# Optimization experiments

Measured on AMD Instinct MI355X. Metric: run time of the kernel, lower is better.

Reference implementation:

```python
import jax, jax.numpy as jnp
import numpy as np

SIZE = 768
SMALL = SIZE // 4 + 1  # 193
N_ROWS = 16 * 512      # 8192 flattened timesteps
N_CODES = 30000
N_PAIRS = 300000


def setup_inputs() -> dict:
    key = jax.random.key(0)
    ks = jax.random.split(key, 10)
    rnn_output = jax.random.normal(ks[0], (16, 512, SIZE), dtype=jnp.float32)
    weight = jax.random.normal(ks[1], (N_CODES, SIZE + 1), dtype=jnp.float32) * 0.02
    weight1 = jax.random.normal(ks[2], (N_CODES, SMALL), dtype=jnp.float32) * 0.02
    idx0 = jnp.stack([
        jax.random.randint(ks[3], (N_PAIRS,), 0, N_ROWS),
        jax.random.randint(ks[4], (N_PAIRS,), 0, N_CODES),
    ], axis=1).astype(jnp.int64)
    y0 = (jax.random.uniform(ks[5], (N_PAIRS,)) < 0.5).astype(jnp.float32)
    idx1 = jnp.stack([
        jax.random.randint(ks[6], (N_PAIRS,), 0, N_ROWS),
        jax.random.randint(ks[7], (N_PAIRS,), 0, N_CODES),
    ], axis=1).astype(jnp.int64)
    y1 = (jax.random.uniform(ks[8], (N_PAIRS,)) < 0.5).astype(jnp.float32)
    seen0 = jnp.zeros((N_PAIRS,), dtype=jnp.float32)
    seen1 = jnp.zeros((N_PAIRS,), dtype=jnp.float32)
    return {"rnn_output": rnn_output, "weight": weight, "weight1": weight1,
            "idx0": idx0, "y0": y0, "seen0": seen0,
            "idx1": idx1, "y1": y1, "seen1": seen1}


def _embedding_dot(features, table, idx):
    # gather feature rows and code-embedding rows, then row-wise dot -> [N]
    f = features[idx[:, 0]]   # [N, D]
    w = table[idx[:, 1]]      # [N, D]
    return jnp.sum(f * w, axis=-1)


def _bce_logits_sum(logits, targets):
    # stable: log(1 + exp(x)) - x*y, summed
    return jnp.sum(jnp.logaddexp(jnp.float32(0.0), logits) - logits * targets)


def reference(rnn_output, weight, weight1, idx0, y0, seen0, idx1, y1, seen1):
    flat = rnn_output.reshape(-1, SIZE)                     # [B*T, size]
    bias = jnp.ones((flat.shape[0], 1), dtype=flat.dtype)
    rnn_with_bias = jnp.concatenate([flat, bias], axis=1)   # [B*T, size+1]

    final = _embedding_dot(rnn_with_bias, weight, idx0)     # [N]
    loss = _bce_logits_sum(final, y0)

    smaller = rnn_with_bias[:, -SMALL:]                     # [B*T, small]
    final1 = _embedding_dot(smaller, weight1, idx1)         # [N]
    loss1 = _bce_logits_sum(final1, y1)

    return final, loss + loss1
```

## Files before the change

kernel.cpp:

```cpp
#include <hip/hip_runtime.h>
#include <hip/hip_fp16.h>

#define FSIZE   768
#define TW0     769
#define TW1     193
#define COL1    576
#define NPAIRS  300000
#define NCODES  30000
#define NROWS   8192
#define NCB     32768

#define NWAVES0 (NPAIRS / 32)
#define NB0     2344
#define NB1     1176
#define NGRID   (NB0 + NB1)
#define NPART   NGRID

#define NBF     3072
#define NBW0    11250
#define NBW1    2813
#define NBH     2344
#define PRE_S1  (NBF)
#define PRE_S2  (NBF + NBW0)
#define PRE_S3  (NBF + NBW0 + NBW1)
#define NPRE    (NBF + NBW0 + NBW1 + NBH)

#define O_FEAT8  ((size_t)0)
#define O_W08    (O_FEAT8 + 1572864)
#define O_W18    (O_W08 + 5760000)
#define O_B0F    (O_W18 + 1440000)
#define O_B1F    (O_B0F + 30000)
#define O_CNT    (O_B1F + 30000)
#define O_CUR    (O_CNT + 65536)
#define O_SREC   (O_CUR + 65536)
#define O_PART   (O_SREC + 2400000)
#define WS_U32   (O_PART + NPART + 64)

#define FSCALE   16.0f
#define WSCALE   64.0f
#define DESCALE  (1.0f / 1024.0f)

typedef float f32x2_t __attribute__((ext_vector_type(2)));

__device__ __forceinline__ float loss_term(float x, float y) {
    float ax = fabsf(x);
    return fmaxf(x, 0.0f) + log1pf(__expf(-ax)) - x * y;
}

__device__ __forceinline__ float4 ld4u(const float* p) {
    float4 v; __builtin_memcpy(&v, p, 16); return v;
}

#if defined(__has_builtin)
# if __has_builtin(__builtin_amdgcn_cvt_pk_f32_fp8)
#  define HW_FP8_DEC 1
# endif
# if __has_builtin(__builtin_amdgcn_cvt_pk_fp8_f32)
#  define HW_FP8_ENC 1
# endif
#endif

__device__ __forceinline__ float sw_fp8_to_f32(unsigned b) {
    unsigned mag = b & 0x7fu;
    unsigned r = ((b & 0x80u) << 24) | ((mag << 20) + 0x3C000000u);
    float f = __uint_as_float(r);
    return mag ? f : 0.0f;
}

template <bool HI>
__device__ __forceinline__ f32x2_t fp8x2_to_f32(unsigned u) {
#ifdef HW_FP8_DEC
    return __builtin_amdgcn_cvt_pk_f32_fp8(u, HI);
#else
    f32x2_t o;
    unsigned lo8 = HI ? ((u >> 16) & 0xffu) : (u & 0xffu);
    unsigned hi8 = HI ? ((u >> 24) & 0xffu) : ((u >> 8) & 0xffu);
    o[0] = sw_fp8_to_f32(lo8);
    o[1] = sw_fp8_to_f32(hi8);
    return o;
#endif
}

__device__ __forceinline__ unsigned sw_f32_to_fp8(float x) {
    unsigned short h = __half_as_ushort(__float2half(x));
    unsigned s = ((unsigned)h >> 8) & 0x80u;
    int e = (h >> 10) & 31;
    unsigned m = h & 1023u;
    if (e >= 23) return s | 0x7eu;
    if (e < 9)  return s;
    unsigned t = ((unsigned)(e - 8) << 3) | (m >> 7);
    unsigned rnd = (m >> 6) & 1u, sticky = (m & 63u) ? 1u : 0u;
    t += (rnd & (sticky | (t & 1u)));
    if (t > 0x7eu) t = 0x7eu;
    return s | t;
}

__device__ __forceinline__ unsigned f32x4_to_fp8(float a, float b, float c, float d) {
#ifdef HW_FP8_ENC
    int u = __builtin_amdgcn_cvt_pk_fp8_f32(a, b, 0, false);
    u = __builtin_amdgcn_cvt_pk_fp8_f32(c, d, u, true);
    return (unsigned)u;
#else
    return sw_f32_to_fp8(a) | (sw_f32_to_fp8(b) << 8)
         | (sw_f32_to_fp8(c) << 16) | (sw_f32_to_fp8(d) << 24);
#endif
}

__device__ __forceinline__ float dot16(uint4 u, const float* w, float s) {
    f32x2_t p;
    p = fp8x2_to_f32<false>(u.x); s += p[0] * w[0]  + p[1] * w[1];
    p = fp8x2_to_f32<true >(u.x); s += p[0] * w[2]  + p[1] * w[3];
    p = fp8x2_to_f32<false>(u.y); s += p[0] * w[4]  + p[1] * w[5];
    p = fp8x2_to_f32<true >(u.y); s += p[0] * w[6]  + p[1] * w[7];
    p = fp8x2_to_f32<false>(u.z); s += p[0] * w[8]  + p[1] * w[9];
    p = fp8x2_to_f32<true >(u.z); s += p[0] * w[10] + p[1] * w[11];
    p = fp8x2_to_f32<false>(u.w); s += p[0] * w[12] + p[1] * w[13];
    p = fp8x2_to_f32<true >(u.w); s += p[0] * w[14] + p[1] * w[15];
    return s;
}

__device__ __forceinline__ float dot8(uint2 u, const float* w, float s) {
    f32x2_t p;
    p = fp8x2_to_f32<false>(u.x); s += p[0] * w[0] + p[1] * w[1];
    p = fp8x2_to_f32<true >(u.x); s += p[0] * w[2] + p[1] * w[3];
    p = fp8x2_to_f32<false>(u.y); s += p[0] * w[4] + p[1] * w[5];
    p = fp8x2_to_f32<true >(u.y); s += p[0] * w[6] + p[1] * w[7];
    return s;
}

__device__ __forceinline__ void unpack16(uint4 u, float* w) {
    f32x2_t p;
    p = fp8x2_to_f32<false>(u.x); w[0]  = p[0]; w[1]  = p[1];
    p = fp8x2_to_f32<true >(u.x); w[2]  = p[0]; w[3]  = p[1];
    p = fp8x2_to_f32<false>(u.y); w[4]  = p[0]; w[5]  = p[1];
    p = fp8x2_to_f32<true >(u.y); w[6]  = p[0]; w[7]  = p[1];
    p = fp8x2_to_f32<false>(u.z); w[8]  = p[0]; w[9]  = p[1];
    p = fp8x2_to_f32<true >(u.z); w[10] = p[0]; w[11] = p[1];
    p = fp8x2_to_f32<false>(u.w); w[12] = p[0]; w[13] = p[1];
    p = fp8x2_to_f32<true >(u.w); w[14] = p[0]; w[15] = p[1];
}

__device__ __forceinline__ void unpack8(uint2 u, float* w) {
    f32x2_t p;
    p = fp8x2_to_f32<false>(u.x); w[0] = p[0]; w[1] = p[1];
    p = fp8x2_to_f32<true >(u.x); w[2] = p[0]; w[3] = p[1];
    p = fp8x2_to_f32<false>(u.y); w[4] = p[0]; w[5] = p[1];
    p = fp8x2_to_f32<true >(u.y); w[6] = p[0]; w[7] = p[1];
}

__global__ __launch_bounds__(256) void zero_cnt_kernel(int* __restrict__ cnt) {
    cnt[blockIdx.x * 256 + threadIdx.x] = 0;
}

__global__ __launch_bounds__(256) void fused_pre_kernel(
    const float* __restrict__ feat, const float* __restrict__ w0,
    const float* __restrict__ w1,
    const int* __restrict__ idx0, const int* __restrict__ idx1,
    uint2* __restrict__ feat8, uint2* __restrict__ w08, uint2* __restrict__ w18,
    float* __restrict__ b0f, float* __restrict__ b1f, int* __restrict__ cnt)
{
    const int bid = blockIdx.x;
    if (bid < PRE_S1) {
        const int t = bid * 256 + threadIdx.x;
        const float* src = feat + (size_t)t * 8;
        float4 a = *(const float4*)src, b = *(const float4*)(src + 4);
        uint2 o;
        o.x = f32x4_to_fp8(a.x * FSCALE, a.y * FSCALE, a.z * FSCALE, a.w * FSCALE);
        o.y = f32x4_to_fp8(b.x * FSCALE, b.y * FSCALE, b.z * FSCALE, b.w * FSCALE);
        feat8[t] = o;
    } else if (bid < PRE_S2) {
        const int t = (bid - PRE_S1) * 256 + threadIdx.x;
        const int c = t / 96;
        const int e = (t - c * 96) * 8;
        const float* src = w0 + (size_t)c * TW0 + e;
        float4 a = ld4u(src), b = ld4u(src + 4);
        uint2 o;
        o.x = f32x4_to_fp8(a.x * WSCALE, a.y * WSCALE, a.z * WSCALE, a.w * WSCALE);
        o.y = f32x4_to_fp8(b.x * WSCALE, b.y * WSCALE, b.z * WSCALE, b.w * WSCALE);
        w08[t] = o;
        if (e == 0) b0f[c] = w0[(size_t)c * TW0 + FSIZE];
    } else if (bid < PRE_S3) {
        const int t = (bid - PRE_S2) * 256 + threadIdx.x;
        if (t < NCODES * 24) {
            const int c = t / 24;
            const int e = (t - c * 24) * 8;
            const float* src = w1 + (size_t)c * TW1 + e;
            float4 a = ld4u(src), b = ld4u(src + 4);
            uint2 o;
            o.x = f32x4_to_fp8(a.x * WSCALE, a.y * WSCALE, a.z * WSCALE, a.w * WSCALE);
            o.y = f32x4_to_fp8(b.x * WSCALE, b.y * WSCALE, b.z * WSCALE, b.w * WSCALE);
            w18[t] = o;
            if (e == 0) b1f[c] = w1[(size_t)c * TW1 + (TW1 - 1)];
        }
    } else {
        const int t = (bid - PRE_S3) * 256 + threadIdx.x;
        if (t < 2 * NPAIRS) {
            if (t < NPAIRS) atomicAdd(&cnt[idx0[2 * t + 1]], 1);
            else            atomicAdd(&cnt[NCB + idx1[2 * (t - NPAIRS) + 1]], 1);
        }
    }
}

__global__ __launch_bounds__(1024) void scan2_kernel(const int* __restrict__ cnt,
                                                     int* __restrict__ cursor) {
    __shared__ int wsum[16];
    __shared__ int wbase[16];
    const int t = threadIdx.x;
    const int lane = t & 63, wv = t >> 6;
    const int4* c4 = (const int4*)cnt + (size_t)t * 16;
    int4 v[16];
#pragma unroll
    for (int j = 0; j < 16; ++j) v[j] = c4[j];
    int s = 0;
#pragma unroll
    for (int j = 0; j < 16; ++j) {
        int a;
        a = v[j].x; v[j].x = s; s += a;
        a = v[j].y; v[j].y = s; s += a;
        a = v[j].z; v[j].z = s; s += a;
        a = v[j].w; v[j].w = s; s += a;
    }
    int incl = s;
#pragma unroll
    for (int off = 1; off < 64; off <<= 1) {
        int u = __shfl_up(incl, off, 64);
        if (lane >= off) incl += u;
    }
    if (lane == 63) wsum[wv] = incl;
    __syncthreads();
    if (wv == 0 && lane < 16) {
        int mysum = wsum[lane];
        int winc = mysum;
#pragma unroll
        for (int off = 1; off < 16; off <<= 1) {
            int u = __shfl_up(winc, off, 64);
            if (lane >= off) winc += u;
        }
        wbase[lane] = winc - mysum;
    }
    __syncthreads();
    const int base = wbase[wv] + incl - s;
    int4* cu = (int4*)cursor + (size_t)t * 16;
#pragma unroll
    for (int j = 0; j < 16; ++j)
        cu[j] = make_int4(base + v[j].x, base + v[j].y, base + v[j].z, base + v[j].w);
}

__global__ __launch_bounds__(256) void scatter2_kernel(
    const int* __restrict__ idx0, const float* __restrict__ y0,
    const int* __restrict__ idx1, const float* __restrict__ y1,
    int* __restrict__ cursor, uint4* __restrict__ srec)
{
    const int t = blockIdx.x * 256 + threadIdx.x;
    if (t < NPAIRS) {
        int r = idx0[2 * t], c = idx0[2 * t + 1];
        int pos = atomicAdd(&cursor[c], 1);
        srec[pos] = make_uint4((unsigned)r, (unsigned)c, __float_as_uint(y0[t]), (unsigned)t);
    } else if (t < 2 * NPAIRS) {
        int p = t - NPAIRS;
        int r = idx1[2 * p], c = idx1[2 * p + 1];
        int pos = atomicAdd(&cursor[NCB + c], 1);
        srec[pos] = make_uint4((unsigned)r, (unsigned)c, __float_as_uint(y1[p]), (unsigned)p);
    }
}

__global__ __launch_bounds__(256) void main3_kernel(
    const unsigned char* __restrict__ feat8, const unsigned char* __restrict__ w08,
    const unsigned char* __restrict__ w18,
    const float* __restrict__ b0f, const float* __restrict__ b1f,
    const uint4* __restrict__ srec,
    float* __restrict__ out_final, float* __restrict__ partial)
{
    __shared__ float bsum[4];
    const int lane = threadIdx.x & 63;
    const int wv   = threadIdx.x >> 6;
    float wavesum = 0.f;

    if (blockIdx.x < NB0) {
        const int work = (blockIdx.x & 7) * (NB0 / 8) + (blockIdx.x >> 3);
        const int wid = work * 4 + wv;
        if (wid < NWAVES0) {
            const int g = lane >> 4, sub = lane & 15;
            const uint4 rec = srec[(size_t)wid * 32 + 8 * g + (sub & 7)];
            int prev_c = -1;
            float wc[48];
            float wb = 0.f, lg = 0.f;
#pragma unroll
            for (int j = 0; j < 8; ++j) {
                const int src = (lane & 48) | j;
                const int r = __shfl((int)rec.x, src, 64);
                const int c = __shfl((int)rec.y, src, 64);
                if (c != prev_c) {
                    prev_c = c;
                    const unsigned char* wr = w08 + (size_t)c * FSIZE + 48 * sub;
                    uint4 wu0 = *(const uint4*)wr;
                    uint4 wu1 = *(const uint4*)(wr + 16);
                    uint4 wu2 = *(const uint4*)(wr + 32);
                    unpack16(wu0, &wc[0]);
                    unpack16(wu1, &wc[16]);
                    unpack16(wu2, &wc[32]);
                    wb = b0f[c];
                }
                const unsigned char* fr = feat8 + (size_t)r * FSIZE + 48 * sub;
                uint4 f0 = *(const uint4*)fr;
                uint4 f1 = *(const uint4*)(fr + 16);
                uint4 f2 = *(const uint4*)(fr + 32);
                float s = dot16(f0, &wc[0], 0.f);
                s = dot16(f1, &wc[16], s);
                s = dot16(f2, &wc[32], s);
                s += __shfl_xor(s, 8, 64);
                s += __shfl_xor(s, 4, 64);
                s += __shfl_xor(s, 2, 64);
                s += __shfl_xor(s, 1, 64);
                lg = (sub == j) ? s * DESCALE + wb : lg;
            }
            float ll = 0.f;
            if (sub < 8) {
                out_final[rec.w] = lg;
                ll = loss_term(lg, __uint_as_float(rec.z));
            }
#pragma unroll
            for (int m = 32; m; m >>= 1) ll += __shfl_xor(ll, m, 64);
            wavesum = ll;
        }
    } else {
        const int tb = blockIdx.x - NB0;
        const int work1 = (tb & 7) * (NB1 / 8) + (tb >> 3);
        const long base = (long)(work1 * 4 + wv) * 64;
        if (base < NPAIRS) {
            const int g = lane >> 3, sub = lane & 7;
            long lpos = base + 8 * g + sub;
            if (lpos > NPAIRS - 1) lpos = NPAIRS - 1;
            const uint4 rec = srec[(size_t)NPAIRS + lpos];
            int prev_c = -1;
            float wc[24];
            float wb = 0.f, lg = 0.f;
#pragma unroll
            for (int j = 0; j < 8; ++j) {
                const bool valid = (base + 8 * g + j) < NPAIRS;
                const int src = (lane & 56) | j;
                const int r = __shfl((int)rec.x, src, 64);
                const int c = __shfl((int)rec.y, src, 64);
                if (valid) {
                    if (c != prev_c) {
                        prev_c = c;
                        const unsigned char* wr = w18 + (size_t)c * 192 + 24 * sub;
                        uint2 wu0 = *(const uint2*)wr;
                        uint2 wu1 = *(const uint2*)(wr + 8);
                        uint2 wu2 = *(const uint2*)(wr + 16);
                        unpack8(wu0, &wc[0]);
                        unpack8(wu1, &wc[8]);
                        unpack8(wu2, &wc[16]);
                        wb = b1f[c];
                    }
                    const unsigned char* fr = feat8 + (size_t)r * FSIZE + COL1 + 24 * sub;
                    uint2 f0 = *(const uint2*)fr;
                    uint2 f1 = *(const uint2*)(fr + 8);
                    uint2 f2 = *(const uint2*)(fr + 16);
                    float s = dot8(f0, &wc[0], 0.f);
                    s = dot8(f1, &wc[8], s);
                    s = dot8(f2, &wc[16], s);
                    s += __shfl_xor(s, 4, 64);
                    s += __shfl_xor(s, 2, 64);
                    s += __shfl_xor(s, 1, 64);
                    lg = (sub == j) ? s * DESCALE + wb : lg;
                }
            }
            float ll = 0.f;
            if ((base + 8 * g + sub) < NPAIRS)
                ll = loss_term(lg, __uint_as_float(rec.z));
#pragma unroll
            for (int m = 32; m; m >>= 1) ll += __shfl_xor(ll, m, 64);
            wavesum = ll;
        }
    }

    if (lane == 0) bsum[wv] = wavesum;
    __syncthreads();
    if (threadIdx.x == 0)
        partial[blockIdx.x] = bsum[0] + bsum[1] + bsum[2] + bsum[3];
}

__global__ __launch_bounds__(1024) void reduce_kernel(
    const float* __restrict__ partial, int n, float* __restrict__ out)
{
    __shared__ float sh[1024];
    float s = 0.0f;
    for (int i = threadIdx.x; i < n; i += 1024) s += partial[i];
    sh[threadIdx.x] = s;
    __syncthreads();
    for (int off = 512; off; off >>= 1) {
        if ((int)threadIdx.x < off) sh[threadIdx.x] += sh[threadIdx.x + off];
        __syncthreads();
    }
    if (threadIdx.x == 0) out[0] = sh[0];
}

__global__ __launch_bounds__(256) void task0_kernel(
    const float* __restrict__ feat, const float* __restrict__ wt,
    const int* __restrict__ idx, const float* __restrict__ y,
    float* __restrict__ out_final, float* __restrict__ partial)
{
    __shared__ float lsum[4];
    const int lane = threadIdx.x & 63;
    const int wv = threadIdx.x >> 6;
    const int pair = blockIdx.x * 4 + wv;
    const int r = idx[2 * pair];
    const int c = idx[2 * pair + 1];
    const float4* f4 = (const float4*)(feat + (size_t)r * FSIZE);
    const float* wrow = wt + (size_t)c * TW0;
    float s = 0.0f;
#pragma unroll
    for (int k = 0; k < 3; ++k) {
        const int j = lane + (k << 6);
        float4 f = f4[j];
        float4 w = ld4u(wrow + 4 * j);
        s += f.x * w.x + f.y * w.y + f.z * w.z + f.w * w.w;
    }
#pragma unroll
    for (int m = 32; m; m >>= 1) s += __shfl_xor(s, m, 64);
    if (lane == 0) {
        const float logit = s + wrow[FSIZE];
        out_final[pair] = logit;
        lsum[wv] = loss_term(logit, y[pair]);
    }
    __syncthreads();
    if (threadIdx.x == 0)
        partial[blockIdx.x] = lsum[0] + lsum[1] + lsum[2] + lsum[3];
}

__global__ __launch_bounds__(256) void task1_kernel(
    const float* __restrict__ feat, const float* __restrict__ wt,
    const int* __restrict__ idx, const float* __restrict__ y,
    float* __restrict__ partial)
{
    __shared__ float lsum[16];
    const int lane = threadIdx.x & 63;
    const int wv = threadIdx.x >> 6;
    const int sub = lane & 15;
    const int pg = lane >> 4;
    const int pair = (blockIdx.x * 4 + wv) * 4 + pg;
    const int r = idx[2 * pair];
    const int c = idx[2 * pair + 1];
    const float4* f4 = (const float4*)(feat + (size_t)r * FSIZE + COL1);
    const float* wrow = wt + (size_t)c * TW1;
    float s = 0.0f;
#pragma unroll
    for (int k = 0; k < 3; ++k) {
        const int j = sub + (k << 4);
        float4 f = f4[j];
        float4 w = ld4u(wrow + 4 * j);
        s += f.x * w.x + f.y * w.y + f.z * w.z + f.w * w.w;
    }
#pragma unroll
    for (int m = 8; m; m >>= 1) s += __shfl_xor(s, m, 64);
    if (sub == 0) {
        const float logit = s + wrow[TW1 - 1];
        lsum[wv * 4 + pg] = loss_term(logit, y[pair]);
    }
    __syncthreads();
    if (threadIdx.x == 0) {
        float t = 0.0f;
#pragma unroll
        for (int i = 0; i < 16; ++i) t += lsum[i];
        partial[blockIdx.x] = t;
    }
}

extern "C" void kernel_launch(void* const* d_in, const int* in_sizes, int n_in,
                              void* d_out, int out_size, void* d_ws, size_t ws_size,
                              hipStream_t stream) {
    const float* feat = (const float*)d_in[0];
    const float* w0   = (const float*)d_in[1];
    const float* w1   = (const float*)d_in[2];
    const int*   idx0 = (const int*)d_in[3];
    const float* y0   = (const float*)d_in[4];
    const int*   idx1 = (const int*)d_in[6];
    const float* y1   = (const float*)d_in[7];

    float* out = (float*)d_out;
    unsigned* ws = (unsigned*)d_ws;

    if (ws_size >= WS_U32 * 4) {
        unsigned char* feat8 = (unsigned char*)(ws + O_FEAT8);
        unsigned char* w08   = (unsigned char*)(ws + O_W08);
        unsigned char* w18   = (unsigned char*)(ws + O_W18);
        float* b0f   = (float*)(ws + O_B0F);
        float* b1f   = (float*)(ws + O_B1F);
        int*   cnt   = (int*)(ws + O_CNT);
        int*   cursor= (int*)(ws + O_CUR);
        uint4* srec  = (uint4*)(ws + O_SREC);
        float* part  = (float*)(ws + O_PART);

        zero_cnt_kernel<<<256, 256, 0, stream>>>(cnt);
        fused_pre_kernel<<<NPRE, 256, 0, stream>>>(
            feat, w0, w1, idx0, idx1,
            (uint2*)feat8, (uint2*)w08, (uint2*)w18, b0f, b1f, cnt);
        scan2_kernel<<<1, 1024, 0, stream>>>(cnt, cursor);
        scatter2_kernel<<<(2 * NPAIRS + 255) / 256, 256, 0, stream>>>(
            idx0, y0, idx1, y1, cursor, srec);
        main3_kernel<<<NGRID, 256, 0, stream>>>(
            feat8, w08, w18, b0f, b1f, srec, out, part);
        reduce_kernel<<<1, 1024, 0, stream>>>(part, NPART, out + NPAIRS);
    } else {
        float* part = (float*)ws;
        const int nb0 = NPAIRS / 4;
        const int nb1 = NPAIRS / 16;
        task0_kernel<<<nb0, 256, 0, stream>>>(feat, w0, idx0, y0, out, part);
        task1_kernel<<<nb1, 256, 0, stream>>>(feat, w1, idx1, y1, part + nb0);
        reduce_kernel<<<1, 1024, 0, stream>>>(part, nb0 + nb1, out + NPAIRS);
    }
}
```

Measured before the change: 161.3 us.

## Widen fp8 packing, grid-stride prep kernels, enlarge task0 waves, fold loss reduce into atomics

The prep kernel now encodes 16 values per thread into uint4 and uses a fixed, smaller grid with per-thread loops, and the histogram section is moved first. The scatter kernel also uses grid-stride loops and zeroes the loss output. The task0 path in main3 now has each wave handle 64 pairs with all 16 lanes per group active, which halves its block count. The final reduce kernel is removed and replaced by per-block atomicAdd into the loss. Together these cut launch count and block scheduling overhead, at the cost of higher register pressure and a nondeterministic float summation order.

```diff
diff --git a/kernel.cpp b/kernel.cpp
--- a/kernel.cpp
+++ b/kernel.cpp
@@ -10,20 +10,22 @@
 #define NROWS   8192
 #define NCB     32768
 
-#define NWAVES0 (NPAIRS / 32)
-#define NB0     2344
+#define NB0     1176
 #define NB1     1176
 #define NGRID   (NB0 + NB1)
 #define NPART   NGRID
 
-#define NBF     3072
-#define NBW0    11250
-#define NBW1    2813
-#define NBH     2344
-#define PRE_S1  (NBF)
-#define PRE_S2  (NBF + NBW0)
-#define PRE_S3  (NBF + NBW0 + NBW1)
-#define NPRE    (NBF + NBW0 + NBW1 + NBH)
+#define PB_H    512
+#define PB_F    512
+#define PB_W0   1024
+#define PB_W1   256
+#define NPRE    (PB_H + PB_F + PB_W0 + PB_W1)
+#define S_H     (PB_H)
+#define S_F     (PB_H + PB_F)
+#define S_W0    (PB_H + PB_F + PB_W0)
+#define FEAT_U4 393216
+#define W0_U4   1440000
+#define W1_U4   360000
 
 #define O_FEAT8  ((size_t)0)
 #define O_W08    (O_FEAT8 + 1572864)
@@ -106,6 +108,16 @@
 #endif
 }
 
+__device__ __forceinline__ uint4 enc16(const float* s, float sc) {
+    float4 a = ld4u(s), b = ld4u(s + 4), c = ld4u(s + 8), d = ld4u(s + 12);
+    uint4 o;
+    o.x = f32x4_to_fp8(a.x * sc, a.y * sc, a.z * sc, a.w * sc);
+    o.y = f32x4_to_fp8(b.x * sc, b.y * sc, b.z * sc, b.w * sc);
+    o.z = f32x4_to_fp8(c.x * sc, c.y * sc, c.z * sc, c.w * sc);
+    o.w = f32x4_to_fp8(d.x * sc, d.y * sc, d.z * sc, d.w * sc);
+    return o;
+}
+
 __device__ __forceinline__ float dot16(uint4 u, const float* w, float s) {
     f32x2_t p;
     p = fp8x2_to_f32<false>(u.x); s += p[0] * w[0]  + p[1] * w[1];
@@ -156,47 +168,52 @@
     const float* __restrict__ feat, const float* __restrict__ w0,
     const float* __restrict__ w1,
     const int* __restrict__ idx0, const int* __restrict__ idx1,
-    uint2* __restrict__ feat8, uint2* __restrict__ w08, uint2* __restrict__ w18,
+    uint4* __restrict__ feat8, uint4* __restrict__ w08, uint4* __restrict__ w18,
     float* __restrict__ b0f, float* __restrict__ b1f, int* __restrict__ cnt)
 {
     const int bid = blockIdx.x;
-    if (bid < PRE_S1) {
-        const int t = bid * 256 + threadIdx.x;
-        const float* src = feat + (size_t)t * 8;
-        float4 a = *(const float4*)src, b = *(const float4*)(src + 4);
-        uint2 o;
-        o.x = f32x4_to_fp8(a.x * FSCALE, a.y * FSCALE, a.z * FSCALE, a.w * FSCALE);
-        o.y = f32x4_to_fp8(b.x * FSCALE, b.y * FSCALE, b.z * FSCALE, b.w * FSCALE);
-        feat8[t] = o;
-    } else if (bid < PRE_S2) {
-        const int t = (bid - PRE_S1) * 256 + threadIdx.x;
-        const int c = t / 96;
-        const int e = (t - c * 96) * 8;
-        const float* src = w0 + (size_t)c * TW0 + e;
-        float4 a = ld4u(src), b = ld4u(src + 4);
-        uint2 o;
-        o.x = f32x4_to_fp8(a.x * WSCALE, a.y * WSCALE, a.z * WSCALE, a.w * WSCALE);
-        o.y = f32x4_to_fp8(b.x * WSCALE, b.y * WSCALE, b.z * WSCALE, b.w * WSCALE);
-        w08[t] = o;
-        if (e == 0) b0f[c] = w0[(size_t)c * TW0 + FSIZE];
-    } else if (bid < PRE_S3) {
-        const int t = (bid - PRE_S2) * 256 + threadIdx.x;
-        if (t < NCODES * 24) {
-            const int c = t / 24;
-            const int e = (t - c * 24) * 8;
-            const float* src = w1 + (size_t)c * TW1 + e;
-            float4 a = ld4u(src), b = ld4u(src + 4);
-            uint2 o;
-            o.x = f32x4_to_fp8(a.x * WSCALE, a.y * WSCALE, a.z * WSCALE, a.w * WSCALE);
-            o.y = f32x4_to_fp8(b.x * WSCALE, b.y * WSCALE, b.z * WSCALE, b.w * WSCALE);
-            w18[t] = o;
-            if (e == 0) b1f[c] = w1[(size_t)c * TW1 + (TW1 - 1)];
+    if (bid < S_H) {
+        const int tid = bid * 256 + threadIdx.x;
+#pragma unroll
+        for (int k = 0; k < 5; ++k) {
+            const int i = tid + k * (PB_H * 256);
+            if (i < 2 * NPAIRS) {
+                if (i < NPAIRS) atomicAdd(&cnt[idx0[2 * i + 1]], 1);
+                else            atomicAdd(&cnt[NCB + idx1[2 * (i - NPAIRS) + 1]], 1);
+            }
+        }
+    } else if (bid < S_F) {
+        const int tid = (bid - S_H) * 256 + threadIdx.x;
+#pragma unroll
+        for (int k = 0; k < 3; ++k) {
+            const int i = tid + k * (PB_F * 256);
+            feat8[i] = enc16(feat + (size_t)i * 16, FSCALE);
+        }
+    } else if (bid < S_W0) {
+        const int tid = (bid - S_F) * 256 + threadIdx.x;
+#pragma unroll
+        for (int k = 0; k < 6; ++k) {
+            const int i = tid + k * (PB_W0 * 256);
+            if (i < W0_U4) {
+                const int c = i / 48;
+                const int e = (i - c * 48) * 16;
+                const float* src = w0 + (size_t)c * TW0 + e;
+                w08[i] = enc16(src, WSCALE);
+                if (e == 0) b0f[c] = src[FSIZE];
+            }
         }
     } else {
-        const int t = (bid - PRE_S3) * 256 + threadIdx.x;
-        if (t < 2 * NPAIRS) {
-            if (t < NPAIRS) atomicAdd(&cnt[idx0[2 * t + 1]], 1);
-            else            atomicAdd(&cnt[NCB + idx1[2 * (t - NPAIRS) + 1]], 1);
+        const int tid = (bid - S_W0) * 256 + threadIdx.x;
+#pragma unroll
+        for (int k = 0; k < 6; ++k) {
+            const int i = tid + k * (PB_W1 * 256);
+            if (i < W1_U4) {
+                const int c = i / 12;
+                const int e = (i - c * 12) * 16;
+                const float* src = w1 + (size_t)c * TW1 + e;
+                w18[i] = enc16(src, WSCALE);
+                if (e == 0) b1f[c] = src[TW1 - 1];
+            }
         }
     }
 }
@@ -249,18 +266,23 @@
 __global__ __launch_bounds__(256) void scatter2_kernel(
     const int* __restrict__ idx0, const float* __restrict__ y0,
     const int* __restrict__ idx1, const float* __restrict__ y1,
-    int* __restrict__ cursor, uint4* __restrict__ srec)
+    int* __restrict__ cursor, uint4* __restrict__ srec, float* __restrict__ loss_out)
 {
-    const int t = blockIdx.x * 256 + threadIdx.x;
-    if (t < NPAIRS) {
-        int r = idx0[2 * t], c = idx0[2 * t + 1];
-        int pos = atomicAdd(&cursor[c], 1);
-        srec[pos] = make_uint4((unsigned)r, (unsigned)c, __float_as_uint(y0[t]), (unsigned)t);
-    } else if (t < 2 * NPAIRS) {
-        int p = t - NPAIRS;
-        int r = idx1[2 * p], c = idx1[2 * p + 1];
-        int pos = atomicAdd(&cursor[NCB + c], 1);
-        srec[pos] = make_uint4((unsigned)r, (unsigned)c, __float_as_uint(y1[p]), (unsigned)p);
+    const int tid = blockIdx.x * 256 + threadIdx.x;
+    if (tid == 0) loss_out[0] = 0.0f;
+#pragma unroll
+    for (int k = 0; k < 2; ++k) {
+        const int t = tid + k * 300032;
+        if (t < NPAIRS) {
+            int r = idx0[2 * t], c = idx0[2 * t + 1];
+            int pos = atomicAdd(&cursor[c], 1);
+            srec[pos] = make_uint4((unsigned)r, (unsigned)c, __float_as_uint(y0[t]), (unsigned)t);
+        } else if (t < 2 * NPAIRS) {
+            int p = t - NPAIRS;
+            int r = idx1[2 * p], c = idx1[2 * p + 1];
+            int pos = atomicAdd(&cursor[NCB + c], 1);
+            srec[pos] = make_uint4((unsigned)r, (unsigned)c, __float_as_uint(y1[p]), (unsigned)p);
+        }
     }
 }
 
@@ -269,7 +291,7 @@
     const unsigned char* __restrict__ w18,
     const float* __restrict__ b0f, const float* __restrict__ b1f,
     const uint4* __restrict__ srec,
-    float* __restrict__ out_final, float* __restrict__ partial)
+    float* __restrict__ out_final, float* __restrict__ loss_out)
 {
     __shared__ float bsum[4];
     const int lane = threadIdx.x & 63;
@@ -279,14 +301,17 @@
     if (blockIdx.x < NB0) {
         const int work = (blockIdx.x & 7) * (NB0 / 8) + (blockIdx.x >> 3);
         const int wid = work * 4 + wv;
-        if (wid < NWAVES0) {
-            const int g = lane >> 4, sub = lane & 15;
-            const uint4 rec = srec[(size_t)wid * 32 + 8 * g + (sub & 7)];
-            int prev_c = -1;
-            float wc[48];
-            float wb = 0.f, lg = 0.f;
-#pragma unroll
-            for (int j = 0; j < 8; ++j) {
+        const int g = lane >> 4, sub = lane & 15;
+        const int mypair = wid * 64 + 16 * g + sub;
+        int rdidx = mypair < NPAIRS ? mypair : NPAIRS - 1;
+        const uint4 rec = srec[rdidx];
+        int prev_c = -1;
+        float wc[48];
+        float wb = 0.f, lg = 0.f;
+#pragma unroll
+        for (int j = 0; j < 16; ++j) {
+            const bool valid = (wid * 64 + 16 * g + j) < NPAIRS;
+            if (valid) {
                 const int src = (lane & 48) | j;
                 const int r = __shfl((int)rec.x, src, 64);
                 const int c = __shfl((int)rec.y, src, 64);
@@ -314,15 +339,15 @@
                 s += __shfl_xor(s, 1, 64);
                 lg = (sub == j) ? s * DESCALE + wb : lg;
             }
-            float ll = 0.f;
-            if (sub < 8) {
-                out_final[rec.w] = lg;
-                ll = loss_term(lg, __uint_as_float(rec.z));
-            }
-#pragma unroll
-            for (int m = 32; m; m >>= 1) ll += __shfl_xor(ll, m, 64);
-            wavesum = ll;
-        }
+        }
+        float ll = 0.f;
+        if (mypair < NPAIRS) {
+            out_final[rec.w] = lg;
+            ll = loss_term(lg, __uint_as_float(rec.z));
+        }
+#pragma unroll
+        for (int m = 32; m; m >>= 1) ll += __shfl_xor(ll, m, 64);
+        wavesum = ll;
     } else {
         const int tb = blockIdx.x - NB0;
         const int work1 = (tb & 7) * (NB1 / 8) + (tb >> 3);
@@ -377,8 +402,10 @@
 
     if (lane == 0) bsum[wv] = wavesum;
     __syncthreads();
-    if (threadIdx.x == 0)
-        partial[blockIdx.x] = bsum[0] + bsum[1] + bsum[2] + bsum[3];
+    if (threadIdx.x == 0) {
+        float t = bsum[0] + bsum[1] + bsum[2] + bsum[3];
+        atomicAdd(loss_out, t);
+    }
 }
 
 __global__ __launch_bounds__(1024) void reduce_kernel(
@@ -490,18 +517,16 @@
         int*   cnt   = (int*)(ws + O_CNT);
         int*   cursor= (int*)(ws + O_CUR);
         uint4* srec  = (uint4*)(ws + O_SREC);
-        float* part  = (float*)(ws + O_PART);
 
         zero_cnt_kernel<<<256, 256, 0, stream>>>(cnt);
         fused_pre_kernel<<<NPRE, 256, 0, stream>>>(
             feat, w0, w1, idx0, idx1,
-            (uint2*)feat8, (uint2*)w08, (uint2*)w18, b0f, b1f, cnt);
+            (uint4*)feat8, (uint4*)w08, (uint4*)w18, b0f, b1f, cnt);
         scan2_kernel<<<1, 1024, 0, stream>>>(cnt, cursor);
-        scatter2_kernel<<<(2 * NPAIRS + 255) / 256, 256, 0, stream>>>(
-            idx0, y0, idx1, y1, cursor, srec);
+        scatter2_kernel<<<1172, 256, 0, stream>>>(
+            idx0, y0, idx1, y1, cursor, srec, out + NPAIRS);
         main3_kernel<<<NGRID, 256, 0, stream>>>(
-            feat8, w08, w18, b0f, b1f, srec, out, part);
-        reduce_kernel<<<1, 1024, 0, stream>>>(part, NPART, out + NPAIRS);
+            feat8, w08, w18, b0f, b1f, srec, out, out + NPAIRS);
     } else {
         float* part = (float*)ws;
         const int nb0 = NPAIRS / 4;
```

Result: slower. 167.5 us (+3.9%).
